# Kernel optimization log

Hardware: AMD Instinct MI355X
Metric: run time of the kernel (lower is better)

The kernel has to match this reference:

```python
import jax, jax.numpy as jnp
import numpy as np

NUM_NODES = 128
TEMPERATURE = 1.0
NEG = -1e30  # stand-in for -inf that is safe under softmax/grad


def setup_inputs() -> dict:
    key = jax.random.key(0)
    k1, k2, k3 = jax.random.split(key, 3)
    D, N = 1024, NUM_NODES
    P = jax.random.normal(k1, (N, N), jnp.float32)
    P = P.at[jnp.arange(N), jnp.arange(N)].set(-50.0)  # fill_diagonal_(-50)
    uniforms = jax.random.uniform(k2, (D, N), jnp.float32)       # categorical sampling draws
    gumbel_u = jax.random.uniform(k3, (D, 2, N, N), jnp.float32)  # gumbel-softmax base uniforms
    return {"P": P, "uniforms": uniforms, "gumbel_u": gumbel_u, "num_dags": D}


def reference(P, uniforms, gumbel_u, num_dags):
    N = P.shape[0]
    D = uniforms.shape[0]
    sigP = jax.nn.sigmoid(P)  # [N,N], shared across all dags

    # --- Phase 1: sequential node-ordering sampling (mask-based, fixed shapes) ---
    def step(active, u):
        # active: [D,N] bool, True = node still remaining
        masked = jnp.where(active[:, None, :], sigP[None, :, :], NEG)  # [D,N,N]
        row_max = masked.max(-1)                                       # max over remaining cols
        logits = jnp.where(active, (1.0 - row_max) / TEMPERATURE, NEG)
        probs = jax.nn.softmax(logits, axis=-1)                        # softmax over remaining rows
        cum = jnp.cumsum(probs, -1)
        cond = (cum >= u[:, None]) & active
        idx = jnp.argmax(cond, -1)
        last_active = (N - 1) - jnp.argmax(active[:, ::-1], -1)
        idx = jnp.where(cond.any(-1), idx, last_active)  # fp fallback
        active = active & (jnp.arange(N)[None, :] != idx[:, None])
        return active, idx

    active0 = jnp.ones((D, N), dtype=bool)
    _, order_T = jax.lax.scan(step, active0, uniforms.T)  # scan over N steps
    order = order_T.T  # [D,N]

    # --- Phase 2: permute, lower-triangular, gumbel-softmax, unpermute ---
    Ap = sigP[order[:, :, None], order[:, None, :]]  # [D,N,N] = sigP[order_i, order_j]
    tril_mask = jnp.tril(jnp.ones((N, N), dtype=bool), -1)
    A_low = jnp.where(tril_mask, Ap, 0.0)
    logA = jnp.where(tril_mask, jnp.log(jnp.where(tril_mask, Ap, 1.0)), NEG)
    log1mA = jnp.log1p(-A_low)
    logits2 = jnp.stack([logA, log1mA], axis=1)  # [D,2,N,N]
    g = -jnp.log(-jnp.log(gumbel_u + 1e-10) + 1e-10)
    y_soft = jax.nn.softmax(logits2 + g, axis=1)  # tau = 1 (torch default)
    am = jnp.argmax(y_soft, axis=1)  # [D,N,N]
    hard = (am[:, None, :, :] == jnp.arange(2)[None, :, None, None]).astype(y_soft.dtype)
    y = jax.lax.stop_gradient(hard - y_soft) + y_soft  # straight-through
    Y = y[:, 0]  # [D,N,N]

    # undo permutation: out[d, order[i], order[j]] = Y[d, i, j]
    inv = jnp.argsort(order, axis=-1)
    unperm = jax.vmap(lambda m, p: m[p][:, p])(Y, inv)
    return unperm.transpose(0, 2, 1), order
```

## Files before the change

kernel.cpp:

```cpp
#include <hip/hip_runtime.h>

#define NN 128
#define NEGF -1e30f
#define DELTA 1.5e-5f

__device__ __forceinline__ float dpp_scan_add(float x) {
    int v;
    v = __builtin_amdgcn_update_dpp(0, __float_as_int(x), 0x111, 0xf, 0xf, true);
    x += __int_as_float(v);
    v = __builtin_amdgcn_update_dpp(0, __float_as_int(x), 0x112, 0xf, 0xf, true);
    x += __int_as_float(v);
    v = __builtin_amdgcn_update_dpp(0, __float_as_int(x), 0x114, 0xf, 0xf, true);
    x += __int_as_float(v);
    v = __builtin_amdgcn_update_dpp(0, __float_as_int(x), 0x118, 0xf, 0xf, true);
    x += __int_as_float(v);
    v = __builtin_amdgcn_update_dpp(0, __float_as_int(x), 0x142, 0xa, 0xf, true);
    x += __int_as_float(v);
    v = __builtin_amdgcn_update_dpp(0, __float_as_int(x), 0x143, 0xc, 0xf, true);
    x += __int_as_float(v);
    return x;
}

__device__ __forceinline__ float dpp_scan_max(float x) {
    const int negi = __float_as_int(NEGF);
    int v;
    v = __builtin_amdgcn_update_dpp(negi, __float_as_int(x), 0x111, 0xf, 0xf, false);
    x = fmaxf(x, __int_as_float(v));
    v = __builtin_amdgcn_update_dpp(negi, __float_as_int(x), 0x112, 0xf, 0xf, false);
    x = fmaxf(x, __int_as_float(v));
    v = __builtin_amdgcn_update_dpp(negi, __float_as_int(x), 0x114, 0xf, 0xf, false);
    x = fmaxf(x, __int_as_float(v));
    v = __builtin_amdgcn_update_dpp(negi, __float_as_int(x), 0x118, 0xf, 0xf, false);
    x = fmaxf(x, __int_as_float(v));
    v = __builtin_amdgcn_update_dpp(negi, __float_as_int(x), 0x142, 0xa, 0xf, false);
    x = fmaxf(x, __int_as_float(v));
    v = __builtin_amdgcn_update_dpp(negi, __float_as_int(x), 0x143, 0xc, 0xf, false);
    x = fmaxf(x, __int_as_float(v));
    return x;
}

__device__ __forceinline__ float bcast63(float x) {
    return __int_as_float(__builtin_amdgcn_readlane(__float_as_int(x), 63));
}

__global__ void k_sig(const float* __restrict__ P, float* __restrict__ sigS) {
    int i = blockIdx.x * blockDim.x + threadIdx.x;
    if (i < NN * NN) {
        double p = (double)P[i];
        sigS[i] = (float)(1.0 / (1.0 + exp(-p)));
    }
}

__launch_bounds__(256)
__global__ void k_fused(const float* __restrict__ sigS,
                        const float* __restrict__ uniforms,
                        const float* __restrict__ G,
                        float* __restrict__ out0,
                        float* __restrict__ orderF, int D) {
    __shared__ float S[NN * NN];
    __shared__ unsigned char T8[4][NN * NN];
    __shared__ int ordS[4 * NN];
    const int tid = threadIdx.x;

    for (int k = 0; k < 16; ++k) {
        int idx4 = (k * 256 + tid) * 4;
        int r = idx4 >> 7, cb = idx4 & 127;
        float4 v = *reinterpret_cast<const float4*>(&sigS[idx4]);
        int x = r & 31;
        float4 w;
        switch (x & 3) {
            case 0: w = v; break;
            case 1: w = make_float4(v.y, v.x, v.w, v.z); break;
            case 2: w = make_float4(v.z, v.w, v.x, v.y); break;
            default: w = make_float4(v.w, v.z, v.y, v.x); break;
        }
        *reinterpret_cast<float4*>(&S[r * 128 + ((cb ^ x) & ~3)]) = w;
    }
    __syncthreads();

    const int lane = tid & 63;
    const int wv = tid >> 6;
    const int dag = blockIdx.x * 4 + wv;
    if (dag >= D) return;

    {
        const int i0 = 2 * lane, i1 = 2 * lane + 1;
        const int x0 = i0 & 31, x1 = i1 & 31;
        const int q0 = x0 & 3, q1 = x1 & 3;
        float2 uu = *reinterpret_cast<const float2*>(&uniforms[dag * NN + i0]);

        unsigned long long mlo = ~0ull, mhi = ~0ull;

        float rm0 = NEGF, rm1 = NEGF;
        int rc0 = 0, rc1 = 0;
        for (int k = 0; k < 32; ++k) {
            int cb = 4 * ((k + lane) & 31);
            float4 a = *reinterpret_cast<const float4*>(&S[i0 * 128 + (cb ^ (x0 & ~3))]);
            float4 b = *reinterpret_cast<const float4*>(&S[i1 * 128 + (cb ^ (x1 & ~3))]);
            if (a.x > rm0) { rm0 = a.x; rc0 = cb | (0 ^ q0); }
            if (a.y > rm0) { rm0 = a.y; rc0 = cb | (1 ^ q0); }
            if (a.z > rm0) { rm0 = a.z; rc0 = cb | (2 ^ q0); }
            if (a.w > rm0) { rm0 = a.w; rc0 = cb | (3 ^ q0); }
            if (b.x > rm1) { rm1 = b.x; rc1 = cb | (0 ^ q1); }
            if (b.y > rm1) { rm1 = b.y; rc1 = cb | (1 ^ q1); }
            if (b.z > rm1) { rm1 = b.z; rc1 = cb | (2 ^ q1); }
            if (b.w > rm1) { rm1 = b.w; rc1 = cb | (3 ^ q1); }
        }

        float e0 = __expf(1.0f - rm0);
        float e1 = __expf(1.0f - rm1);

        #pragma unroll 1
        for (int t = 0; t < NN; ++t) {
            float usel = (t & 1) ? uu.y : uu.x;
            float ut = __int_as_float(__builtin_amdgcn_readlane(__float_as_int(usel), t >> 1));

            float incl = dpp_scan_add(e0 + e1);
            float T = bcast63(incl);
            float thr = ut * T;
            float cum1 = incl, cum0 = incl - e1;

            bool a0 = (e0 != 0.0f), a1 = (e1 != 0.0f);
            bool c0 = a0 && (cum0 >= thr);
            bool c1 = a1 && (cum1 >= thr);
            float mg = DELTA * T;
            bool amb = (a0 && fabsf(cum0 - thr) <= mg) || (a1 && fabsf(cum1 - thr) <= mg);

            unsigned long long b0 = __ballot(c0), b1 = __ballot(c1);
            unsigned long long ba = __ballot(amb);
            int lastActive = mhi ? (127 - __clzll(mhi)) : (63 - __clzll(mlo));

            int idx;
            if (__builtin_expect(ba != 0ull, 0)) {
                float l0 = 1.0f - rm0, l1v = 1.0f - rm1;
                float lvi = fmaxf(a0 ? l0 : NEGF, a1 ? l1v : NEGF);
                float lv = bcast63(dpp_scan_max(lvi));
                float f0 = a0 ? expf(l0 - lv) : 0.0f;
                float f1 = a1 ? expf(l1v - lv) : 0.0f;
                int mm = lane & 3;
                float s0 = __shfl(f0, mm), s1 = __shfl(f1, mm);
                #pragma unroll
                for (int k2 = 1; k2 < 16; ++k2) {
                    s0 += __shfl(f0, mm + 4 * k2);
                    s1 += __shfl(f1, mm + 4 * k2);
                }
                float A00 = __shfl(s0, 0), A01 = __shfl(s0, 1), A02 = __shfl(s0, 2), A03 = __shfl(s0, 3);
                float A10 = __shfl(s1, 0), A11 = __shfl(s1, 1), A12 = __shfl(s1, 2), A13 = __shfl(s1, 3);
                float tot = ((A00 + A10) + (A01 + A11)) + ((A02 + A12) + (A03 + A13));
                float s = 0.0f;
                int pick = -1;
                for (int j = 0; j < NN; ++j) {
                    float ej = __shfl((j & 1) ? f1 : f0, j >> 1);
                    float pj = ej / tot;
                    s += pj;
                    bool aj = (j < 64) ? ((mlo >> j) & 1ull) : ((mhi >> (j - 64)) & 1ull);
                    if (pick < 0 && aj && s >= ut) pick = j;
                }
                idx = (pick >= 0) ? pick : lastActive;
            } else {
                int f0i = b0 ? 2 * (__ffsll(b0) - 1) : 999;
                int f1i = b1 ? 2 * (__ffsll(b1) - 1) + 1 : 999;
                idx = min(f0i, f1i);
                if (idx == 999) idx = lastActive;
            }

            if (lane == 0) ordS[wv * NN + t] = idx;

            if (idx < 64) mlo &= ~(1ull << idx);
            else          mhi &= ~(1ull << (idx - 64));
            if (idx == i0) e0 = 0.0f;
            if (idx == i1) e1 = 0.0f;
            a0 = (e0 != 0.0f); a1 = (e1 != 0.0f);

            unsigned long long r0 = __ballot(a0 && (rc0 == idx));
            unsigned long long r1 = __ballot(a1 && (rc1 == idx));

            while (r0) {
                int L = __ffsll(r0) - 1; r0 &= r0 - 1;
                int row = 2 * L, xm = row & 31;
                float v0 = ((mlo >> lane) & 1) ? S[row * 128 + (lane ^ xm)] : NEGF;
                float v1 = ((mhi >> lane) & 1) ? S[row * 128 + ((lane + 64) ^ xm)] : NEGF;
                float m2 = bcast63(dpp_scan_max(fmaxf(v0, v1)));
                unsigned long long h0 = __ballot(v0 == m2);
                unsigned long long h1 = __ballot(v1 == m2);
                int nc = h0 ? (__ffsll(h0) - 1) : (64 + __ffsll(h1) - 1);
                if (lane == L) { rm0 = m2; rc0 = nc; e0 = __expf(1.0f - m2); }
            }
            while (r1) {
                int L = __ffsll(r1) - 1; r1 &= r1 - 1;
                int row = 2 * L + 1, xm = row & 31;
                float v0 = ((mlo >> lane) & 1) ? S[row * 128 + (lane ^ xm)] : NEGF;
                float v1 = ((mhi >> lane) & 1) ? S[row * 128 + ((lane + 64) ^ xm)] : NEGF;
                float m2 = bcast63(dpp_scan_max(fmaxf(v0, v1)));
                unsigned long long h0 = __ballot(v0 == m2);
                unsigned long long h1 = __ballot(v1 == m2);
                int nc = h0 ? (__ffsll(h0) - 1) : (64 + __ffsll(h1) - 1);
                if (lane == L) { rm1 = m2; rc1 = nc; e1 = __expf(1.0f - m2); }
            }
        }
    }

    const int* pw = &ordS[wv * NN];
    unsigned char* Tw = T8[wv];

    {
        float2 o = make_float2((float)pw[2 * lane], (float)pw[2 * lane + 1]);
        *reinterpret_cast<float2*>(&orderF[(size_t)dag * NN + 2 * lane]) = o;
    }

    uint4 z = make_uint4(0, 0, 0, 0);
    #pragma unroll
    for (int k = 0; k < 16; ++k)
        reinterpret_cast<uint4*>(Tw)[k * 64 + lane] = z;
    asm volatile("s_waitcnt lgkmcnt(0)" ::: "memory");

    const float* G0 = G + (size_t)dag * 2 * NN * NN;
    const float* G1 = G0 + NN * NN;

    for (int base = 0; base < 8192; base += 512) {
        float u0[8], u1[8], sg[8];
        int rr8[8], cc8[8];
        bool ok[8];
        #pragma unroll
        for (int j = 0; j < 8; ++j) {
            int k = base + j * 64 + lane;
            ok[j] = (k < 8128);
            if (ok[j]) {
                float fr = sqrtf(8.0f * (float)k + 1.0f);
                int r = (int)((1.0f + fr) * 0.5f);
                if (r * (r - 1) / 2 > k) --r;
                if ((r + 1) * r / 2 <= k) ++r;
                int c = k - r * (r - 1) / 2;
                rr8[j] = r; cc8[j] = c;
                int idx = r * NN + c;
                u0[j] = G0[idx];
                u1[j] = G1[idx];
                int prr = pw[r], pcc = pw[c];
                sg[j] = S[prr * 128 + (pcc ^ (prr & 31))];
            }
        }
        #pragma unroll
        for (int j = 0; j < 8; ++j) {
            if (ok[j]) {
                int prr = pw[rr8[j]], pcc = pw[cc8[j]];
                float A = -__logf(u0[j] + 1e-10f) + 1e-10f;
                float B = -__logf(u1[j] + 1e-10f) + 1e-10f;
                Tw[pcc * NN + (prr ^ (pcc & 124))] = (sg[j] * B >= (1.0f - sg[j]) * A) ? 1 : 0;
            }
        }
    }

    float* od = out0 + (size_t)dag * NN * NN;
    #pragma unroll 4
    for (int k = 0; k < 64; ++k) {
        int base = k * 256 + lane * 4;
        int i = base >> 7, j = base & 127;
        const uchar4 v = *reinterpret_cast<const uchar4*>(&Tw[i * NN + (j ^ (i & 124))]);
        float4 o;
        o.x = (float)v.x; o.y = (float)v.y; o.z = (float)v.z; o.w = (float)v.w;
        *reinterpret_cast<float4*>(&od[base]) = o;
    }
}

extern "C" void kernel_launch(void* const* d_in, const int* in_sizes, int n_in,
                              void* d_out, int out_size, void* d_ws, size_t ws_size,
                              hipStream_t stream) {
    const float* P        = (const float*)d_in[0];
    const float* uniforms = (const float*)d_in[1];
    const float* G        = (const float*)d_in[2];
    const int D = in_sizes[1] / NN;

    float* out0   = (float*)d_out;
    float* orderF = out0 + (size_t)D * NN * NN;
    float* sigS   = (float*)d_ws;

    k_sig<<<(NN * NN + 255) / 256, 256, 0, stream>>>(P, sigS);
    k_fused<<<(D + 3) / 4, 256, 0, stream>>>(sigS, uniforms, G, out0, orderF, D);
}
```

Baseline: 157.8 us.

## Interleave gumbel edge computation for previous row into sequential ordering loop

Moves the phase-2 gumbel-softmax edge evaluation into the sequential sampling loop. At step t it loads and computes row t-1 of the permuted lower triangle, since that row's order entries are already known, and finishes the last row after the loop. The aim is to hide global loads of the gumbel uniforms and the log math behind the latency-bound serial sampling chain, and to drop the separate triangular-index pass with its sqrt. The cost is extra register pressure and memory traffic inside the serial loop, which could lengthen each step.

```diff
diff --git a/kernel.cpp b/kernel.cpp
--- a/kernel.cpp
+++ b/kernel.cpp
@@ -83,170 +83,189 @@
     const int dag = blockIdx.x * 4 + wv;
     if (dag >= D) return;
 
+    unsigned char* Tw = T8[wv];
     {
-        const int i0 = 2 * lane, i1 = 2 * lane + 1;
-        const int x0 = i0 & 31, x1 = i1 & 31;
-        const int q0 = x0 & 3, q1 = x1 & 3;
-        float2 uu = *reinterpret_cast<const float2*>(&uniforms[dag * NN + i0]);
-
-        unsigned long long mlo = ~0ull, mhi = ~0ull;
-
-        float rm0 = NEGF, rm1 = NEGF;
-        int rc0 = 0, rc1 = 0;
-        for (int k = 0; k < 32; ++k) {
-            int cb = 4 * ((k + lane) & 31);
-            float4 a = *reinterpret_cast<const float4*>(&S[i0 * 128 + (cb ^ (x0 & ~3))]);
-            float4 b = *reinterpret_cast<const float4*>(&S[i1 * 128 + (cb ^ (x1 & ~3))]);
-            if (a.x > rm0) { rm0 = a.x; rc0 = cb | (0 ^ q0); }
-            if (a.y > rm0) { rm0 = a.y; rc0 = cb | (1 ^ q0); }
-            if (a.z > rm0) { rm0 = a.z; rc0 = cb | (2 ^ q0); }
-            if (a.w > rm0) { rm0 = a.w; rc0 = cb | (3 ^ q0); }
-            if (b.x > rm1) { rm1 = b.x; rc1 = cb | (0 ^ q1); }
-            if (b.y > rm1) { rm1 = b.y; rc1 = cb | (1 ^ q1); }
-            if (b.z > rm1) { rm1 = b.z; rc1 = cb | (2 ^ q1); }
-            if (b.w > rm1) { rm1 = b.w; rc1 = cb | (3 ^ q1); }
-        }
-
-        float e0 = __expf(1.0f - rm0);
-        float e1 = __expf(1.0f - rm1);
-
-        #pragma unroll 1
-        for (int t = 0; t < NN; ++t) {
-            float usel = (t & 1) ? uu.y : uu.x;
-            float ut = __int_as_float(__builtin_amdgcn_readlane(__float_as_int(usel), t >> 1));
-
-            float incl = dpp_scan_add(e0 + e1);
-            float T = bcast63(incl);
-            float thr = ut * T;
-            float cum1 = incl, cum0 = incl - e1;
-
-            bool a0 = (e0 != 0.0f), a1 = (e1 != 0.0f);
-            bool c0 = a0 && (cum0 >= thr);
-            bool c1 = a1 && (cum1 >= thr);
-            float mg = DELTA * T;
-            bool amb = (a0 && fabsf(cum0 - thr) <= mg) || (a1 && fabsf(cum1 - thr) <= mg);
-
-            unsigned long long b0 = __ballot(c0), b1 = __ballot(c1);
-            unsigned long long ba = __ballot(amb);
-            int lastActive = mhi ? (127 - __clzll(mhi)) : (63 - __clzll(mlo));
-
-            int idx;
-            if (__builtin_expect(ba != 0ull, 0)) {
-                float l0 = 1.0f - rm0, l1v = 1.0f - rm1;
-                float lvi = fmaxf(a0 ? l0 : NEGF, a1 ? l1v : NEGF);
-                float lv = bcast63(dpp_scan_max(lvi));
-                float f0 = a0 ? expf(l0 - lv) : 0.0f;
-                float f1 = a1 ? expf(l1v - lv) : 0.0f;
-                int mm = lane & 3;
-                float s0 = __shfl(f0, mm), s1 = __shfl(f1, mm);
-                #pragma unroll
-                for (int k2 = 1; k2 < 16; ++k2) {
-                    s0 += __shfl(f0, mm + 4 * k2);
-                    s1 += __shfl(f1, mm + 4 * k2);
-                }
-                float A00 = __shfl(s0, 0), A01 = __shfl(s0, 1), A02 = __shfl(s0, 2), A03 = __shfl(s0, 3);
-                float A10 = __shfl(s1, 0), A11 = __shfl(s1, 1), A12 = __shfl(s1, 2), A13 = __shfl(s1, 3);
-                float tot = ((A00 + A10) + (A01 + A11)) + ((A02 + A12) + (A03 + A13));
-                float s = 0.0f;
-                int pick = -1;
-                for (int j = 0; j < NN; ++j) {
-                    float ej = __shfl((j & 1) ? f1 : f0, j >> 1);
-                    float pj = ej / tot;
-                    s += pj;
-                    bool aj = (j < 64) ? ((mlo >> j) & 1ull) : ((mhi >> (j - 64)) & 1ull);
-                    if (pick < 0 && aj && s >= ut) pick = j;
-                }
-                idx = (pick >= 0) ? pick : lastActive;
-            } else {
-                int f0i = b0 ? 2 * (__ffsll(b0) - 1) : 999;
-                int f1i = b1 ? 2 * (__ffsll(b1) - 1) + 1 : 999;
-                idx = min(f0i, f1i);
-                if (idx == 999) idx = lastActive;
+        uint4 z = make_uint4(0, 0, 0, 0);
+        #pragma unroll
+        for (int k = 0; k < 16; ++k)
+            reinterpret_cast<uint4*>(Tw)[k * 64 + lane] = z;
+        asm volatile("s_waitcnt lgkmcnt(0)" ::: "memory");
+    }
+
+    const float* G0 = G + (size_t)dag * 2 * NN * NN;
+    const float* G1 = G0 + NN * NN;
+
+    const int i0 = 2 * lane, i1 = 2 * lane + 1;
+    const int x0 = i0 & 31, x1 = i1 & 31;
+    const int q0 = x0 & 3, q1 = x1 & 3;
+    float2 uu = *reinterpret_cast<const float2*>(&uniforms[dag * NN + i0]);
+
+    unsigned long long mlo = ~0ull, mhi = ~0ull;
+
+    float rm0 = NEGF, rm1 = NEGF;
+    int rc0 = 0, rc1 = 0;
+    for (int k = 0; k < 32; ++k) {
+        int cb = 4 * ((k + lane) & 31);
+        float4 a = *reinterpret_cast<const float4*>(&S[i0 * 128 + (cb ^ (x0 & ~3))]);
+        float4 b = *reinterpret_cast<const float4*>(&S[i1 * 128 + (cb ^ (x1 & ~3))]);
+        if (a.x > rm0) { rm0 = a.x; rc0 = cb | (0 ^ q0); }
+        if (a.y > rm0) { rm0 = a.y; rc0 = cb | (1 ^ q0); }
+        if (a.z > rm0) { rm0 = a.z; rc0 = cb | (2 ^ q0); }
+        if (a.w > rm0) { rm0 = a.w; rc0 = cb | (3 ^ q0); }
+        if (b.x > rm1) { rm1 = b.x; rc1 = cb | (0 ^ q1); }
+        if (b.y > rm1) { rm1 = b.y; rc1 = cb | (1 ^ q1); }
+        if (b.z > rm1) { rm1 = b.z; rc1 = cb | (2 ^ q1); }
+        if (b.w > rm1) { rm1 = b.w; rc1 = cb | (3 ^ q1); }
+    }
+
+    float e0 = __expf(1.0f - rm0);
+    float e1 = __expf(1.0f - rm1);
+
+    int pidx = 0;
+    int pc0 = 0, pc1 = 0;
+
+    #pragma unroll 1
+    for (int t = 0; t < NN; ++t) {
+        const int rrow = t - 1;
+        const bool k0 = (rrow >= 1) && (lane < rrow);
+        const bool k1 = (rrow >= 1) && (lane + 64 < rrow);
+        float u00 = 0.0f, u10 = 0.0f, u01 = 0.0f, u11 = 0.0f, sg0 = 0.0f, sg1 = 0.0f;
+        if (k0) {
+            u00 = G0[rrow * NN + lane];
+            u10 = G1[rrow * NN + lane];
+            sg0 = S[pidx * 128 + (pc0 ^ (pidx & 31))];
+        }
+        if (k1) {
+            u01 = G0[rrow * NN + 64 + lane];
+            u11 = G1[rrow * NN + 64 + lane];
+            sg1 = S[pidx * 128 + (pc1 ^ (pidx & 31))];
+        }
+
+        float usel = (t & 1) ? uu.y : uu.x;
+        float ut = __int_as_float(__builtin_amdgcn_readlane(__float_as_int(usel), t >> 1));
+
+        float incl = dpp_scan_add(e0 + e1);
+        float T = bcast63(incl);
+        float thr = ut * T;
+        float cum1 = incl, cum0 = incl - e1;
+
+        bool a0 = (e0 != 0.0f), a1 = (e1 != 0.0f);
+        bool c0 = a0 && (cum0 >= thr);
+        bool c1 = a1 && (cum1 >= thr);
+        float mg = DELTA * T;
+        bool amb = (a0 && fabsf(cum0 - thr) <= mg) || (a1 && fabsf(cum1 - thr) <= mg);
+
+        unsigned long long b0 = __ballot(c0), b1 = __ballot(c1);
+        unsigned long long ba = __ballot(amb);
+        int lastActive = mhi ? (127 - __clzll(mhi)) : (63 - __clzll(mlo));
+
+        int idx;
+        if (__builtin_expect(ba != 0ull, 0)) {
+            float l0 = 1.0f - rm0, l1v = 1.0f - rm1;
+            float lvi = fmaxf(a0 ? l0 : NEGF, a1 ? l1v : NEGF);
+            float lv = bcast63(dpp_scan_max(lvi));
+            float f0 = a0 ? expf(l0 - lv) : 0.0f;
+            float f1 = a1 ? expf(l1v - lv) : 0.0f;
+            int mm = lane & 3;
+            float s0 = __shfl(f0, mm), s1 = __shfl(f1, mm);
+            #pragma unroll
+            for (int k2 = 1; k2 < 16; ++k2) {
+                s0 += __shfl(f0, mm + 4 * k2);
+                s1 += __shfl(f1, mm + 4 * k2);
             }
-
-            if (lane == 0) ordS[wv * NN + t] = idx;
-
-            if (idx < 64) mlo &= ~(1ull << idx);
-            else          mhi &= ~(1ull << (idx - 64));
-            if (idx == i0) e0 = 0.0f;
-            if (idx == i1) e1 = 0.0f;
-            a0 = (e0 != 0.0f); a1 = (e1 != 0.0f);
-
-            unsigned long long r0 = __ballot(a0 && (rc0 == idx));
-            unsigned long long r1 = __ballot(a1 && (rc1 == idx));
-
-            while (r0) {
-                int L = __ffsll(r0) - 1; r0 &= r0 - 1;
-                int row = 2 * L, xm = row & 31;
-                float v0 = ((mlo >> lane) & 1) ? S[row * 128 + (lane ^ xm)] : NEGF;
-                float v1 = ((mhi >> lane) & 1) ? S[row * 128 + ((lane + 64) ^ xm)] : NEGF;
-                float m2 = bcast63(dpp_scan_max(fmaxf(v0, v1)));
-                unsigned long long h0 = __ballot(v0 == m2);
-                unsigned long long h1 = __ballot(v1 == m2);
-                int nc = h0 ? (__ffsll(h0) - 1) : (64 + __ffsll(h1) - 1);
-                if (lane == L) { rm0 = m2; rc0 = nc; e0 = __expf(1.0f - m2); }
+            float A00 = __shfl(s0, 0), A01 = __shfl(s0, 1), A02 = __shfl(s0, 2), A03 = __shfl(s0, 3);
+            float A10 = __shfl(s1, 0), A11 = __shfl(s1, 1), A12 = __shfl(s1, 2), A13 = __shfl(s1, 3);
+            float tot = ((A00 + A10) + (A01 + A11)) + ((A02 + A12) + (A03 + A13));
+            float s = 0.0f;
+            int pick = -1;
+            for (int j = 0; j < NN; ++j) {
+                float ej = __shfl((j & 1) ? f1 : f0, j >> 1);
+                float pj = ej / tot;
+                s += pj;
+                bool aj = (j < 64) ? ((mlo >> j) & 1ull) : ((mhi >> (j - 64)) & 1ull);
+                if (pick < 0 && aj && s >= ut) pick = j;
             }
-            while (r1) {
-                int L = __ffsll(r1) - 1; r1 &= r1 - 1;
-                int row = 2 * L + 1, xm = row & 31;
-                float v0 = ((mlo >> lane) & 1) ? S[row * 128 + (lane ^ xm)] : NEGF;
-                float v1 = ((mhi >> lane) & 1) ? S[row * 128 + ((lane + 64) ^ xm)] : NEGF;
-                float m2 = bcast63(dpp_scan_max(fmaxf(v0, v1)));
-                unsigned long long h0 = __ballot(v0 == m2);
-                unsigned long long h1 = __ballot(v1 == m2);
-                int nc = h0 ? (__ffsll(h0) - 1) : (64 + __ffsll(h1) - 1);
-                if (lane == L) { rm1 = m2; rc1 = nc; e1 = __expf(1.0f - m2); }
-            }
-        }
-    }
-
-    const int* pw = &ordS[wv * NN];
-    unsigned char* Tw = T8[wv];
+            idx = (pick >= 0) ? pick : lastActive;
+        } else {
+            int f0i = b0 ? 2 * (__ffsll(b0) - 1) : 999;
+            int f1i = b1 ? 2 * (__ffsll(b1) - 1) + 1 : 999;
+            idx = min(f0i, f1i);
+            if (idx == 999) idx = lastActive;
+        }
+
+        if (lane == 0) ordS[wv * NN + t] = idx;
+
+        if (idx < 64) mlo &= ~(1ull << idx);
+        else          mhi &= ~(1ull << (idx - 64));
+        if (idx == i0) e0 = 0.0f;
+        if (idx == i1) e1 = 0.0f;
+        a0 = (e0 != 0.0f); a1 = (e1 != 0.0f);
+
+        unsigned long long r0 = __ballot(a0 && (rc0 == idx));
+        unsigned long long r1 = __ballot(a1 && (rc1 == idx));
+
+        while (r0) {
+            int L = __ffsll(r0) - 1; r0 &= r0 - 1;
+            int row = 2 * L, xm = row & 31;
+            float v0 = ((mlo >> lane) & 1) ? S[row * 128 + (lane ^ xm)] : NEGF;
+            float v1 = ((mhi >> lane) & 1) ? S[row * 128 + ((lane + 64) ^ xm)] : NEGF;
+            float m2 = bcast63(dpp_scan_max(fmaxf(v0, v1)));
+            unsigned long long h0 = __ballot(v0 == m2);
+            unsigned long long h1 = __ballot(v1 == m2);
+            int nc = h0 ? (__ffsll(h0) - 1) : (64 + __ffsll(h1) - 1);
+            if (lane == L) { rm0 = m2; rc0 = nc; e0 = __expf(1.0f - m2); }
+        }
+        while (r1) {
+            int L = __ffsll(r1) - 1; r1 &= r1 - 1;
+            int row = 2 * L + 1, xm = row & 31;
+            float v0 = ((mlo >> lane) & 1) ? S[row * 128 + (lane ^ xm)] : NEGF;
+            float v1 = ((mhi >> lane) & 1) ? S[row * 128 + ((lane + 64) ^ xm)] : NEGF;
+            float m2 = bcast63(dpp_scan_max(fmaxf(v0, v1)));
+            unsigned long long h0 = __ballot(v0 == m2);
+            unsigned long long h1 = __ballot(v1 == m2);
+            int nc = h0 ? (__ffsll(h0) - 1) : (64 + __ffsll(h1) - 1);
+            if (lane == L) { rm1 = m2; rc1 = nc; e1 = __expf(1.0f - m2); }
+        }
+
+        if (k0) {
+            float A = -__logf(u00 + 1e-10f) + 1e-10f;
+            float B = -__logf(u10 + 1e-10f) + 1e-10f;
+            Tw[pc0 * NN + (pidx ^ (pc0 & 124))] = (sg0 * B >= (1.0f - sg0) * A) ? 1 : 0;
+        }
+        if (k1) {
+            float A = -__logf(u01 + 1e-10f) + 1e-10f;
+            float B = -__logf(u11 + 1e-10f) + 1e-10f;
+            Tw[pc1 * NN + (pidx ^ (pc1 & 124))] = (sg1 * B >= (1.0f - sg1) * A) ? 1 : 0;
+        }
+
+        if (t == lane)      pc0 = idx;
+        if (t == lane + 64) pc1 = idx;
+        pidx = idx;
+    }
 
     {
+        const int* pw = &ordS[wv * NN];
         float2 o = make_float2((float)pw[2 * lane], (float)pw[2 * lane + 1]);
         *reinterpret_cast<float2*>(&orderF[(size_t)dag * NN + 2 * lane]) = o;
     }
 
-    uint4 z = make_uint4(0, 0, 0, 0);
-    #pragma unroll
-    for (int k = 0; k < 16; ++k)
-        reinterpret_cast<uint4*>(Tw)[k * 64 + lane] = z;
-    asm volatile("s_waitcnt lgkmcnt(0)" ::: "memory");
-
-    const float* G0 = G + (size_t)dag * 2 * NN * NN;
-    const float* G1 = G0 + NN * NN;
-
-    for (int base = 0; base < 8192; base += 512) {
-        float u0[8], u1[8], sg[8];
-        int rr8[8], cc8[8];
-        bool ok[8];
-        #pragma unroll
-        for (int j = 0; j < 8; ++j) {
-            int k = base + j * 64 + lane;
-            ok[j] = (k < 8128);
-            if (ok[j]) {
-                float fr = sqrtf(8.0f * (float)k + 1.0f);
-                int r = (int)((1.0f + fr) * 0.5f);
-                if (r * (r - 1) / 2 > k) --r;
-                if ((r + 1) * r / 2 <= k) ++r;
-                int c = k - r * (r - 1) / 2;
-                rr8[j] = r; cc8[j] = c;
-                int idx = r * NN + c;
-                u0[j] = G0[idx];
-                u1[j] = G1[idx];
-                int prr = pw[r], pcc = pw[c];
-                sg[j] = S[prr * 128 + (pcc ^ (prr & 31))];
-            }
-        }
-        #pragma unroll
-        for (int j = 0; j < 8; ++j) {
-            if (ok[j]) {
-                int prr = pw[rr8[j]], pcc = pw[cc8[j]];
-                float A = -__logf(u0[j] + 1e-10f) + 1e-10f;
-                float B = -__logf(u1[j] + 1e-10f) + 1e-10f;
-                Tw[pcc * NN + (prr ^ (pcc & 124))] = (sg[j] * B >= (1.0f - sg[j]) * A) ? 1 : 0;
-            }
+    {
+        const int rrow = NN - 1;
+        if (lane < rrow) {
+            float u0 = G0[rrow * NN + lane];
+            float u1v = G1[rrow * NN + lane];
+            float sg = S[pidx * 128 + (pc0 ^ (pidx & 31))];
+            float A = -__logf(u0 + 1e-10f) + 1e-10f;
+            float B = -__logf(u1v + 1e-10f) + 1e-10f;
+            Tw[pc0 * NN + (pidx ^ (pc0 & 124))] = (sg * B >= (1.0f - sg) * A) ? 1 : 0;
+        }
+        if (lane + 64 < rrow) {
+            float u0 = G0[rrow * NN + 64 + lane];
+            float u1v = G1[rrow * NN + 64 + lane];
+            float sg = S[pidx * 128 + (pc1 ^ (pidx & 31))];
+            float A = -__logf(u0 + 1e-10f) + 1e-10f;
+            float B = -__logf(u1v + 1e-10f) + 1e-10f;
+            Tw[pc1 * NN + (pidx ^ (pc1 & 124))] = (sg * B >= (1.0f - sg) * A) ? 1 : 0;
         }
     }
 
```

Measured after the change: 211.2 us. 1.34x slower.
